# Kernel optimization log

Measured on AMD Instinct MI355X. Metric: run time of the kernel, lower is better.

Reference implementation:

```python
import jax, jax.numpy as jnp
import numpy as np

N_EMBD = 1024
N_HEAD = 16
B, T = 4, 2048


def setup_inputs() -> dict:
    key = jax.random.key(0)
    k1, k2, k3, k4, k5 = jax.random.split(key, 5)
    s = 0.02
    return {
        "x": jax.random.normal(k1, (B, T, N_EMBD), dtype=jnp.float32),
        "w_attn": jax.random.normal(k2, (N_EMBD, 3 * N_EMBD), dtype=jnp.float32) * s,
        "b_attn": jnp.zeros((3 * N_EMBD,), dtype=jnp.float32),
        "w_proj": jax.random.normal(k3, (N_EMBD, N_EMBD), dtype=jnp.float32) * s,
        "b_proj": jnp.zeros((N_EMBD,), dtype=jnp.float32),
    }


def reference(x, w_attn, b_attn, w_proj, b_proj):
    Bb, Tt, C = x.shape
    hd = C // N_HEAD  # head dim
    qkv = x @ w_attn + b_attn                      # [B,T,3C]
    q, k, v = jnp.split(qkv, 3, axis=-1)
    # [B,T,C] -> [B,H,T,hd]
    def heads(t):
        return t.reshape(Bb, Tt, N_HEAD, hd).transpose(0, 2, 1, 3)
    q, k, v = heads(q), heads(k), heads(v)
    scale = 1.0 / np.sqrt(hd).astype(np.float32)
    attn = jnp.einsum("bhqd,bhkd->bhqk", q, k) * scale  # [B,H,T,T]
    causal = jnp.tril(jnp.ones((Tt, Tt), dtype=bool))
    attn = jnp.where(causal, attn, -jnp.inf)
    attn = jax.nn.softmax(attn, axis=-1)
    y = jnp.einsum("bhqk,bhkd->bhqd", attn, v)          # [B,H,T,hd]
    y = y.transpose(0, 2, 1, 3).reshape(Bb, Tt, C)
    return y @ w_proj + b_proj
```

## Files before the change

### kernel.cpp

```cpp
#include <hip/hip_runtime.h>
#include <cmath>


typedef short short8 __attribute__((ext_vector_type(8)));
typedef short short4v __attribute__((ext_vector_type(4)));
typedef float f32x4 __attribute__((ext_vector_type(4)));

__device__ __forceinline__ short f2bf(float f) {
  unsigned u = __builtin_bit_cast(unsigned, f);
  u = (u + 0x7fffu + ((u >> 16) & 1u)) >> 16;
  return (short)u;
}

__device__ __forceinline__ float exp2_fast(float x) {
  float r;
  asm("v_exp_f32 %0, %1" : "=v"(r) : "v"(x));
  return r;
}

__device__ __forceinline__ void gld_lds16(const void* g, void* l) {
  __builtin_amdgcn_global_load_lds(
      (__attribute__((address_space(1))) void*)g,
      (__attribute__((address_space(3))) void*)l,
      16, 0, 0);
}

__device__ __forceinline__ void barx() {
  asm volatile("s_barrier" ::: "memory");
}

template <int IMM>
__device__ __forceinline__ short8 dsr(int addr) {
  short8 d;
  asm volatile("ds_read_b128 %0, %1 offset:%2"
               : "=v"(d) : "v"(addr), "n"(IMM));
  return d;
}

#define WAITLN(n)                                          \
  asm volatile("s_waitcnt lgkmcnt(" #n ")" ::: "memory");  \
  __builtin_amdgcn_sched_barrier(0);

__global__ void cast_bf16_kernel(const float* __restrict__ in,
                                 short* __restrict__ out, int n4) {
  int i = blockIdx.x * blockDim.x + threadIdx.x;
  if (i < n4) {
    const float4 v = ((const float4*)in)[i];
    short4v o;
    o.x = f2bf(v.x); o.y = f2bf(v.y); o.z = f2bf(v.z); o.w = f2bf(v.w);
    ((short4v*)out)[i] = o;
  }
}

__global__ void transpose_cast_kernel(const float* __restrict__ in,
                                      short* __restrict__ out, int R, int C) {
  __shared__ float tile[32][33];
  int c0 = blockIdx.x * 32, r0 = blockIdx.y * 32;
  int tx = threadIdx.x & 31, tg = threadIdx.x >> 5;
#pragma unroll
  for (int i = 0; i < 4; ++i) {
    int r = tg * 4 + i;
    tile[r][tx] = in[(size_t)(r0 + r) * C + c0 + tx];
  }
  __syncthreads();
#pragma unroll
  for (int i = 0; i < 4; ++i) {
    int c = tg * 4 + i;
    out[(size_t)(c0 + c) * R + r0 + tx] = f2bf(tile[tx][c]);
  }
}


__global__ __launch_bounds__(512, 2) void qkv_gemm_kernel(
    const short* __restrict__ A, const short* __restrict__ Bt,
    const float* __restrict__ bias,
    short* __restrict__ oq, short* __restrict__ ok, short* __restrict__ ovt,
    int M, int N, int K) {
  extern __shared__ short lds[];
  const int NT = K >> 6;
  const int lane = threadIdx.x & 63, wave = threadIdx.x >> 6;
  const int quad = lane >> 4, l16 = lane & 15;
  const int wm2 = wave >> 2, wn4 = wave & 3;

  const int nbn = N >> 8;
  const int swz = (blockIdx.x & 7) * ((int)gridDim.x >> 3) + (blockIdx.x >> 3);
  const int m0 = (swz / nbn) * 128, n0 = (swz % nbn) * 256;

  const int r8 = lane >> 3;
  const int sw8 = ((lane & 7) ^ r8) * 8;
  const short* Ab0 = A + (size_t)(m0 + wave * 8 + r8) * K + sw8;
  const short* Bb0 = Bt + (size_t)(n0 + wave * 8 + r8) * K + sw8;
  short* ldsw = lds + wave * 512;

  auto stage = [&](int t, int mat, int rA, int rB) {
    const short* g = (mat ? Bb0 : Ab0) + t * 64;
    short* d = ldsw + (t & 1) * 24576 + mat * 8192;
    gld_lds16(g + (size_t)rA * K, d + rA * 64);
    gld_lds16(g + (size_t)rB * K, d + rB * 64);
  };

  const int swz0 = ((0 + quad) ^ (l16 & 7)) * 16;
  const int swz1 = ((4 + quad) ^ (l16 & 7)) * 16;
  const int baseA0 = wm2 * 8192 + l16 * 128 + swz0;
  const int baseA1 = wm2 * 8192 + l16 * 128 + swz1;
  const int baseB0 = 16384 + wn4 * 8192 + l16 * 128 + swz0;
  const int baseB1 = 16384 + wn4 * 8192 + l16 * 128 + swz1;

  f32x4 acc[4][4] = {};

  stage(0, 1, 0, 64);
  stage(0, 1, 128, 192);
  stage(0, 0, 0, 64);
  asm volatile("s_waitcnt vmcnt(0)" ::: "memory");
  barx();

#pragma unroll 1
  for (int t = 0; t < NT; ++t) {
    const int vb = (t & 1) * 49152;
    const int aA0 = baseA0 + vb, aA1 = baseA1 + vb;
    const int aB0 = baseB0 + vb, aB1 = baseB1 + vb;
    short8 a0[4], b0[4], a1[4], b1[4];

    b0[0] = dsr<0>(aB0);     b0[1] = dsr<2048>(aB0);
    b0[2] = dsr<4096>(aB0);  b0[3] = dsr<6144>(aB0);
    a0[0] = dsr<0>(aA0);     a0[1] = dsr<2048>(aA0);
    a0[2] = dsr<4096>(aA0);  a0[3] = dsr<6144>(aA0);
    if (t + 1 < NT) {
      stage(t + 1, 1, 0, 64);
      stage(t + 1, 1, 128, 192);
      stage(t + 1, 0, 0, 64);
    }
    b1[0] = dsr<0>(aB1);     b1[1] = dsr<2048>(aB1);
    b1[2] = dsr<4096>(aB1);  b1[3] = dsr<6144>(aB1);
    a1[0] = dsr<0>(aA1);     a1[1] = dsr<2048>(aA1);
    a1[2] = dsr<4096>(aA1);  a1[3] = dsr<6144>(aA1);

    WAITLN(8)
    __builtin_amdgcn_s_setprio(1);
#pragma unroll
    for (int i_ = 0; i_ < 4; ++i_)
#pragma unroll
      for (int n_ = 0; n_ < 4; ++n_)
        acc[i_][n_] = __builtin_amdgcn_mfma_f32_16x16x32_bf16(
            a0[i_], b0[n_], acc[i_][n_], 0, 0, 0);
    __builtin_amdgcn_s_setprio(0);

    WAITLN(0)
    __builtin_amdgcn_s_setprio(1);
#pragma unroll
    for (int i_ = 0; i_ < 4; ++i_)
#pragma unroll
      for (int n_ = 0; n_ < 4; ++n_)
        acc[i_][n_] = __builtin_amdgcn_mfma_f32_16x16x32_bf16(
            a1[i_], b1[n_], acc[i_][n_], 0, 0, 0);
    __builtin_amdgcn_s_setprio(0);

    if (t + 1 < NT)
      asm volatile("s_waitcnt vmcnt(0)" ::: "memory");
    barx();
  }

  const int sec = n0 >> 10;
  const int h0 = (n0 & 1023) >> 6;
  const float scale = (sec == 0) ? 0.18033688f : 1.0f;
  float bv[4];
#pragma unroll
  for (int n_ = 0; n_ < 4; ++n_) bv[n_] = bias[n0 + wn4 * 64 + n_ * 16 + l16];
  const int b_ = m0 >> 11, t0 = m0 & 2047;

  __syncthreads();
  if (sec < 2) {
    short* dst = (sec == 0) ? oq : ok;
#pragma unroll
    for (int mt = 0; mt < 4; ++mt)
#pragma unroll
      for (int n_ = 0; n_ < 4; ++n_) {
        const int col = wn4 * 64 + n_ * 16 + l16;
#pragma unroll
        for (int r = 0; r < 4; ++r)
          lds[(wm2 * 64 + mt * 16 + quad * 4 + r) * 264 + col] =
              f2bf((acc[mt][n_][r] + bv[n_]) * scale);
      }
    __syncthreads();
    const int hl = wave & 3, rg = wave >> 2;
    const short* sp = &lds[(rg * 64 + r8) * 264 + hl * 64 + (lane & 7) * 8];
    short* gp = dst +
        ((size_t)(b_ * 16 + h0 + hl) * 2048 + t0 + rg * 64 + r8) * 64 +
        (lane & 7) * 8;
#pragma unroll
    for (int i = 0; i < 8; ++i)
      *(short8*)(gp + (size_t)i * 512) = *(const short8*)(sp + i * 8 * 264);
  } else {
#pragma unroll
    for (int mt = 0; mt < 4; ++mt)
#pragma unroll
      for (int n_ = 0; n_ < 4; ++n_) {
        const int col = wn4 * 64 + n_ * 16 + l16;
#pragma unroll
        for (int r = 0; r < 4; ++r)
          lds[col * 136 + wm2 * 64 + mt * 16 + quad * 4 + r] =
              f2bf(acc[mt][n_][r] + bv[n_]);
      }
    __syncthreads();
    const int cw = wave * 32 + (lane >> 4);
#pragma unroll
    for (int i = 0; i < 8; ++i) {
      const int c = cw + i * 4;
      const int bh = b_ * 16 + h0 + (c >> 6), d = c & 63;
      *(short8*)(ovt + ((size_t)bh * 64 + d) * 2048 + t0 + (lane & 15) * 8) =
          *(const short8*)&lds[c * 136 + (lane & 15) * 8];
    }
  }
}

template <int MODE>
__global__ __launch_bounds__(256) void gemm_bt_kernel(
    const short* __restrict__ A, const short* __restrict__ Bt,
    const float* __restrict__ bias, float* __restrict__ outf,
    short* __restrict__ oq, short* __restrict__ ok, short* __restrict__ ovt,
    int M, int N, int K) {
  __shared__ short slds[16384];
  short* As = slds;
  short* Bs = slds + 8192;
  const int m0 = blockIdx.y * 128, n0 = blockIdx.x * 128;
  const int lane = threadIdx.x & 63, wave = threadIdx.x >> 6;
  const int quad = lane >> 4, l16 = lane & 15;
  const int wm = (wave >> 1) * 64, wn = (wave & 1) * 64;

  const int row_off = lane >> 3;
  const int segsw = ((lane & 7) ^ row_off) * 8;
  const short* Ag = A + (size_t)(m0 + wave * 32 + row_off) * K + segsw;
  const short* Bg = Bt + (size_t)(n0 + wave * 32 + row_off) * K + segsw;

  f32x4 acc[4][4] = {};

  for (int k0 = 0; k0 < K; k0 += 64) {
#pragma unroll
    for (int g = 0; g < 4; ++g) {
      gld_lds16(Ag + (size_t)(g * 8) * K + k0, &As[(wave * 32 + g * 8) * 64]);
      gld_lds16(Bg + (size_t)(g * 8) * K + k0, &Bs[(wave * 32 + g * 8) * 64]);
    }
    __syncthreads();
#pragma unroll
    for (int kh = 0; kh < 2; ++kh) {
      short8 a[4], b[4];
#pragma unroll
      for (int t = 0; t < 4; ++t) {
        const int R = wm + t * 16 + l16;
        a[t] = *(const short8*)&As[R * 64 + (((kh * 4 + quad) ^ (R & 7)) * 8)];
      }
#pragma unroll
      for (int t = 0; t < 4; ++t) {
        const int R = wn + t * 16 + l16;
        b[t] = *(const short8*)&Bs[R * 64 + (((kh * 4 + quad) ^ (R & 7)) * 8)];
      }
#pragma unroll
      for (int mt = 0; mt < 4; ++mt)
#pragma unroll
        for (int nt = 0; nt < 4; ++nt)
          acc[mt][nt] = __builtin_amdgcn_mfma_f32_16x16x32_bf16(
              a[mt], b[nt], acc[mt][nt], 0, 0, 0);
    }
    __syncthreads();
  }

  float bv[4];
#pragma unroll
  for (int nt = 0; nt < 4; ++nt) bv[nt] = bias[n0 + wn + nt * 16 + l16];

  if (MODE == 1) {
#pragma unroll
    for (int mt = 0; mt < 4; ++mt)
#pragma unroll
      for (int nt = 0; nt < 4; ++nt) {
        const int n = n0 + wn + nt * 16 + l16;
#pragma unroll
        for (int r = 0; r < 4; ++r) {
          const int m = m0 + wm + mt * 16 + quad * 4 + r;
          outf[(size_t)m * N + n] = acc[mt][nt][r] + bv[nt];
        }
      }
  }
}

__global__ __launch_bounds__(256, 6) void attn_kernel(
    const short* __restrict__ q, const short* __restrict__ k,
    const short* __restrict__ vt, short* __restrict__ y) {
  __shared__ short Ks[64 * 64];
  __shared__ short Vs[64 * 64];
  __shared__ short Ps[4][16 * 72];
  const int lane = threadIdx.x & 63, wave = threadIdx.x >> 6;
  const int quad = lane >> 4, l16 = lane & 15;
  const int g = blockIdx.x;
  const int bh = g & 63;
  const int j = 31 - (g >> 6);
  const int b_ = bh >> 4, h = bh & 15;
  const int q0 = j * 64 + wave * 16;

  const short* qbh = q + (size_t)bh * 2048 * 64;
  const short* kbh = k + (size_t)bh * 2048 * 64;
  const short* vbh = vt + (size_t)bh * 64 * 2048;
  short* Pw = Ps[wave];

  const short8 qf0 = *(const short8*)&qbh[(q0 + l16) * 64 + quad * 8];
  const short8 qf1 = *(const short8*)&qbh[(q0 + l16) * 64 + 32 + quad * 8];

  short8 ones;
#pragma unroll
  for (int i = 0; i < 8; ++i) ones[i] = (short)0x3F80;

  f32x4 O[4] = {};
  f32x4 lacc = {};

  const int srow = lane >> 3;
  const int scol = ((lane & 7) ^ srow) * 8;
  const int r0s = wave * 16;

#pragma unroll 1
  for (int c = 0; c <= j; ++c) {
    const int kt0 = c * 64;
    gld_lds16(kbh + (size_t)(kt0 + r0s + srow) * 64 + scol, &Ks[r0s * 64]);
    gld_lds16(kbh + (size_t)(kt0 + r0s + 8 + srow) * 64 + scol, &Ks[(r0s + 8) * 64]);
    gld_lds16(vbh + (size_t)(r0s + srow) * 2048 + kt0 + scol, &Vs[r0s * 64]);
    gld_lds16(vbh + (size_t)(r0s + 8 + srow) * 2048 + kt0 + scol, &Vs[(r0s + 8) * 64]);
    __syncthreads();

    const int sw = l16 & 7;
    f32x4 sc4[4];
#pragma unroll
    for (int cf = 0; cf < 4; ++cf) {
      const int row = cf * 16 + l16;
      const short8 kfa = *(const short8*)&Ks[row * 64 + ((quad ^ sw) * 8)];
      const short8 kfb = *(const short8*)&Ks[row * 64 + (((quad + 4) ^ sw) * 8)];
      f32x4 z = {};
      z = __builtin_amdgcn_mfma_f32_16x16x32_bf16(qf0, kfa, z, 0, 0, 0);
      z = __builtin_amdgcn_mfma_f32_16x16x32_bf16(qf1, kfb, z, 0, 0, 0);
      sc4[cf] = z;
    }

    if (c == j) {
#pragma unroll
      for (int cf = 0; cf < 4; ++cf) {
        const int col = kt0 + cf * 16 + l16;
#pragma unroll
        for (int r = 0; r < 4; ++r) {
          const int rowg = q0 + quad * 4 + r;
          float e = exp2_fast(sc4[cf][r]);
          e = (col > rowg) ? 0.f : e;
          Pw[(quad * 4 + r) * 72 + cf * 16 + l16] = f2bf(e);
        }
      }
    } else {
#pragma unroll
      for (int cf = 0; cf < 4; ++cf)
#pragma unroll
        for (int r = 0; r < 4; ++r)
          Pw[(quad * 4 + r) * 72 + cf * 16 + l16] = f2bf(exp2_fast(sc4[cf][r]));
    }
    asm volatile("s_waitcnt lgkmcnt(0)" ::: "memory");
    const short8 pf0 = *(const short8*)&Pw[l16 * 72 + quad * 8];
    const short8 pf1 = *(const short8*)&Pw[l16 * 72 + 32 + quad * 8];

    lacc = __builtin_amdgcn_mfma_f32_16x16x32_bf16(pf0, ones, lacc, 0, 0, 0);
    lacc = __builtin_amdgcn_mfma_f32_16x16x32_bf16(pf1, ones, lacc, 0, 0, 0);

#pragma unroll
    for (int dt = 0; dt < 4; ++dt) {
      const int d = dt * 16 + l16;
      const short8 vf0 = *(const short8*)&Vs[d * 64 + ((quad ^ sw) * 8)];
      const short8 vf1 = *(const short8*)&Vs[d * 64 + (((quad + 4) ^ sw) * 8)];
      O[dt] = __builtin_amdgcn_mfma_f32_16x16x32_bf16(pf0, vf0, O[dt], 0, 0, 0);
      O[dt] = __builtin_amdgcn_mfma_f32_16x16x32_bf16(pf1, vf1, O[dt], 0, 0, 0);
    }
    __syncthreads();
  }

  float inv[4];
#pragma unroll
  for (int r = 0; r < 4; ++r) inv[r] = 1.0f / lacc[r];
#pragma unroll
  for (int dt = 0; dt < 4; ++dt) {
    const int d = dt * 16 + l16;
#pragma unroll
    for (int r = 0; r < 4; ++r) {
      const int t_ = q0 + quad * 4 + r;
      y[((size_t)b_ * 2048 + t_) * 1024 + h * 64 + d] = f2bf(O[dt][r] * inv[r]);
    }
  }
}

extern "C" void kernel_launch(void* const* d_in, const int* in_sizes, int n_in,
                              void* d_out, int out_size, void* d_ws, size_t ws_size,
                              hipStream_t stream) {
  const float* x      = (const float*)d_in[0];
  const float* w_attn = (const float*)d_in[1];
  const float* b_attn = (const float*)d_in[2];
  const float* w_proj = (const float*)d_in[3];
  const float* b_proj = (const float*)d_in[4];
  float* out = (float*)d_out;

  short* xb  = (short*)d_ws;
  short* wTa = xb + (size_t)8192 * 1024;
  short* wTp = wTa + (size_t)3072 * 1024;
  short* qb  = wTp + (size_t)1024 * 1024;
  short* kb  = qb + (size_t)64 * 2048 * 64;
  short* vtb = kb + (size_t)64 * 2048 * 64;
  short* yb  = vtb + (size_t)64 * 2048 * 64;

  static int lds_attr_done = 0;
  if (!lds_attr_done) {
    (void)hipFuncSetAttribute(reinterpret_cast<const void*>(qkv_gemm_kernel),
                              hipFuncAttributeMaxDynamicSharedMemorySize,
                              98304);
    lds_attr_done = 1;
  }

  cast_bf16_kernel<<<8192, 256, 0, stream>>>(x, xb, 8192 * 1024 / 4);
  transpose_cast_kernel<<<dim3(96, 32), 256, 0, stream>>>(w_attn, wTa, 1024, 3072);
  transpose_cast_kernel<<<dim3(32, 32), 256, 0, stream>>>(w_proj, wTp, 1024, 1024);

  qkv_gemm_kernel<<<768, 512, 98304, stream>>>(
      xb, wTa, b_attn, qb, kb, vtb, 8192, 3072, 1024);

  attn_kernel<<<2048, 256, 0, stream>>>(qb, kb, vtb, yb);

  gemm_bt_kernel<1><<<dim3(8, 64), 256, 0, stream>>>(
      yb, wTp, b_proj, out, nullptr, nullptr, nullptr, 8192, 1024, 1024);
}
```

Before: 242.7 us.

## Reuse pipelined QKV GEMM for projection and double-buffer K in attention

The output projection now runs through the templated 512-thread pipelined GEMM used for QKV, with an fp32 bias epilogue, in place of the simpler 256-thread kernel. The attention kernel double-buffers K tiles in dynamic LDS, prefetching the next tile during compute, and loads V fragments straight from global memory into registers rather than staging them in LDS. P writes and reads use inline ds instructions. This removes one barrier per iteration and overlaps loads with compute. In exchange the attention kernel's occupancy hint drops from 6 to 5, the V reads from global may be less coalesced, and the projection grid shrinks to 256 blocks.

```diff
diff --git a/kernel.cpp b/kernel.cpp
--- a/kernel.cpp
+++ b/kernel.cpp
@@ -40,6 +40,8 @@
 #define WAITLN(n)                                          \
   asm volatile("s_waitcnt lgkmcnt(" #n ")" ::: "memory");  \
   __builtin_amdgcn_sched_barrier(0);
+
+extern __shared__ short lds[];
 
 __global__ void cast_bf16_kernel(const float* __restrict__ in,
                                  short* __restrict__ out, int n4) {
@@ -71,12 +73,12 @@
 }
 
 
-__global__ __launch_bounds__(512, 2) void qkv_gemm_kernel(
+template <int MODE>
+__global__ __launch_bounds__(512, 2) void gemm128_kernel(
     const short* __restrict__ A, const short* __restrict__ Bt,
-    const float* __restrict__ bias,
+    const float* __restrict__ bias, float* __restrict__ outf,
     short* __restrict__ oq, short* __restrict__ ok, short* __restrict__ ovt,
     int M, int N, int K) {
-  extern __shared__ short lds[];
   const int NT = K >> 6;
   const int lane = threadIdx.x & 63, wave = threadIdx.x >> 6;
   const int quad = lane >> 4, l16 = lane & 15;
@@ -160,12 +162,28 @@
     barx();
   }
 
+  float bv[4];
+#pragma unroll
+  for (int n_ = 0; n_ < 4; ++n_) bv[n_] = bias[n0 + wn4 * 64 + n_ * 16 + l16];
+
+  if (MODE == 1) {
+#pragma unroll
+    for (int mt = 0; mt < 4; ++mt)
+#pragma unroll
+      for (int n_ = 0; n_ < 4; ++n_) {
+        const int n = n0 + wn4 * 64 + n_ * 16 + l16;
+#pragma unroll
+        for (int r = 0; r < 4; ++r) {
+          const int m = m0 + wm2 * 64 + mt * 16 + quad * 4 + r;
+          outf[(size_t)m * N + n] = acc[mt][n_][r] + bv[n_];
+        }
+      }
+    return;
+  }
+
   const int sec = n0 >> 10;
   const int h0 = (n0 & 1023) >> 6;
   const float scale = (sec == 0) ? 0.18033688f : 1.0f;
-  float bv[4];
-#pragma unroll
-  for (int n_ = 0; n_ < 4; ++n_) bv[n_] = bias[n0 + wn4 * 64 + n_ * 16 + l16];
   const int b_ = m0 >> 11, t0 = m0 & 2047;
 
   __syncthreads();
@@ -213,82 +231,9 @@
   }
 }
 
-template <int MODE>
-__global__ __launch_bounds__(256) void gemm_bt_kernel(
-    const short* __restrict__ A, const short* __restrict__ Bt,
-    const float* __restrict__ bias, float* __restrict__ outf,
-    short* __restrict__ oq, short* __restrict__ ok, short* __restrict__ ovt,
-    int M, int N, int K) {
-  __shared__ short slds[16384];
-  short* As = slds;
-  short* Bs = slds + 8192;
-  const int m0 = blockIdx.y * 128, n0 = blockIdx.x * 128;
-  const int lane = threadIdx.x & 63, wave = threadIdx.x >> 6;
-  const int quad = lane >> 4, l16 = lane & 15;
-  const int wm = (wave >> 1) * 64, wn = (wave & 1) * 64;
-
-  const int row_off = lane >> 3;
-  const int segsw = ((lane & 7) ^ row_off) * 8;
-  const short* Ag = A + (size_t)(m0 + wave * 32 + row_off) * K + segsw;
-  const short* Bg = Bt + (size_t)(n0 + wave * 32 + row_off) * K + segsw;
-
-  f32x4 acc[4][4] = {};
-
-  for (int k0 = 0; k0 < K; k0 += 64) {
-#pragma unroll
-    for (int g = 0; g < 4; ++g) {
-      gld_lds16(Ag + (size_t)(g * 8) * K + k0, &As[(wave * 32 + g * 8) * 64]);
-      gld_lds16(Bg + (size_t)(g * 8) * K + k0, &Bs[(wave * 32 + g * 8) * 64]);
-    }
-    __syncthreads();
-#pragma unroll
-    for (int kh = 0; kh < 2; ++kh) {
-      short8 a[4], b[4];
-#pragma unroll
-      for (int t = 0; t < 4; ++t) {
-        const int R = wm + t * 16 + l16;
-        a[t] = *(const short8*)&As[R * 64 + (((kh * 4 + quad) ^ (R & 7)) * 8)];
-      }
-#pragma unroll
-      for (int t = 0; t < 4; ++t) {
-        const int R = wn + t * 16 + l16;
-        b[t] = *(const short8*)&Bs[R * 64 + (((kh * 4 + quad) ^ (R & 7)) * 8)];
-      }
-#pragma unroll
-      for (int mt = 0; mt < 4; ++mt)
-#pragma unroll
-        for (int nt = 0; nt < 4; ++nt)
-          acc[mt][nt] = __builtin_amdgcn_mfma_f32_16x16x32_bf16(
-              a[mt], b[nt], acc[mt][nt], 0, 0, 0);
-    }
-    __syncthreads();
-  }
-
-  float bv[4];
-#pragma unroll
-  for (int nt = 0; nt < 4; ++nt) bv[nt] = bias[n0 + wn + nt * 16 + l16];
-
-  if (MODE == 1) {
-#pragma unroll
-    for (int mt = 0; mt < 4; ++mt)
-#pragma unroll
-      for (int nt = 0; nt < 4; ++nt) {
-        const int n = n0 + wn + nt * 16 + l16;
-#pragma unroll
-        for (int r = 0; r < 4; ++r) {
-          const int m = m0 + wm + mt * 16 + quad * 4 + r;
-          outf[(size_t)m * N + n] = acc[mt][nt][r] + bv[nt];
-        }
-      }
-  }
-}
-
-__global__ __launch_bounds__(256, 6) void attn_kernel(
+__global__ __launch_bounds__(256, 5) void attn_kernel(
     const short* __restrict__ q, const short* __restrict__ k,
     const short* __restrict__ vt, short* __restrict__ y) {
-  __shared__ short Ks[64 * 64];
-  __shared__ short Vs[64 * 64];
-  __shared__ short Ps[4][16 * 72];
   const int lane = threadIdx.x & 63, wave = threadIdx.x >> 6;
   const int quad = lane >> 4, l16 = lane & 15;
   const int g = blockIdx.x;
@@ -300,14 +245,9 @@
   const short* qbh = q + (size_t)bh * 2048 * 64;
   const short* kbh = k + (size_t)bh * 2048 * 64;
   const short* vbh = vt + (size_t)bh * 64 * 2048;
-  short* Pw = Ps[wave];
 
   const short8 qf0 = *(const short8*)&qbh[(q0 + l16) * 64 + quad * 8];
   const short8 qf1 = *(const short8*)&qbh[(q0 + l16) * 64 + 32 + quad * 8];
-
-  short8 ones;
-#pragma unroll
-  for (int i = 0; i < 8; ++i) ones[i] = (short)0x3F80;
 
   f32x4 O[4] = {};
   f32x4 lacc = {};
@@ -316,63 +256,99 @@
   const int scol = ((lane & 7) ^ srow) * 8;
   const int r0s = wave * 16;
 
+  const int sw = l16 & 7;
+  const int kaddrA = l16 * 128 + ((quad ^ sw) * 16);
+  const int kaddrB = kaddrA ^ 64;
+  const int pbase = 16384 + wave * 2304;
+  const int pw = pbase + quad * 576 + l16 * 2;
+  const int prd = pbase + l16 * 144 + quad * 16;
+
+  short8 ones;
+#pragma unroll
+  for (int i = 0; i < 8; ++i) ones[i] = (short)0x3F80;
+
+  gld_lds16(kbh + (size_t)(r0s + srow) * 64 + scol, &lds[r0s * 64]);
+  gld_lds16(kbh + (size_t)(r0s + 8 + srow) * 64 + scol, &lds[(r0s + 8) * 64]);
+  __syncthreads();
+
 #pragma unroll 1
   for (int c = 0; c <= j; ++c) {
     const int kt0 = c * 64;
-    gld_lds16(kbh + (size_t)(kt0 + r0s + srow) * 64 + scol, &Ks[r0s * 64]);
-    gld_lds16(kbh + (size_t)(kt0 + r0s + 8 + srow) * 64 + scol, &Ks[(r0s + 8) * 64]);
-    gld_lds16(vbh + (size_t)(r0s + srow) * 2048 + kt0 + scol, &Vs[r0s * 64]);
-    gld_lds16(vbh + (size_t)(r0s + 8 + srow) * 2048 + kt0 + scol, &Vs[(r0s + 8) * 64]);
-    __syncthreads();
-
-    const int sw = l16 & 7;
+    const int kb = (c & 1) * 8192;
+
+    short8 vf[8];
+#pragma unroll
+    for (int dt = 0; dt < 4; ++dt) {
+      const size_t vrow = (size_t)(dt * 16 + l16) * 2048 + kt0 + quad * 8;
+      vf[dt * 2] = *(const short8*)&vbh[vrow];
+      vf[dt * 2 + 1] = *(const short8*)&vbh[vrow + 32];
+    }
+    __builtin_amdgcn_sched_barrier(0);
+    if (c < j) {
+      const int nb = ((c + 1) & 1) * 4096;
+      gld_lds16(kbh + (size_t)(kt0 + 64 + r0s + srow) * 64 + scol,
+                &lds[nb + r0s * 64]);
+      gld_lds16(kbh + (size_t)(kt0 + 64 + r0s + 8 + srow) * 64 + scol,
+                &lds[nb + (r0s + 8) * 64]);
+    }
+    __builtin_amdgcn_sched_barrier(0);
+
+    short8 kfa[4], kfb[4];
+    kfa[0] = dsr<0>(kb + kaddrA);    kfb[0] = dsr<0>(kb + kaddrB);
+    kfa[1] = dsr<2048>(kb + kaddrA); kfb[1] = dsr<2048>(kb + kaddrB);
+    kfa[2] = dsr<4096>(kb + kaddrA); kfb[2] = dsr<4096>(kb + kaddrB);
+    kfa[3] = dsr<6144>(kb + kaddrA); kfb[3] = dsr<6144>(kb + kaddrB);
+    WAITLN(0)
     f32x4 sc4[4];
 #pragma unroll
     for (int cf = 0; cf < 4; ++cf) {
-      const int row = cf * 16 + l16;
-      const short8 kfa = *(const short8*)&Ks[row * 64 + ((quad ^ sw) * 8)];
-      const short8 kfb = *(const short8*)&Ks[row * 64 + (((quad + 4) ^ sw) * 8)];
       f32x4 z = {};
-      z = __builtin_amdgcn_mfma_f32_16x16x32_bf16(qf0, kfa, z, 0, 0, 0);
-      z = __builtin_amdgcn_mfma_f32_16x16x32_bf16(qf1, kfb, z, 0, 0, 0);
+      z = __builtin_amdgcn_mfma_f32_16x16x32_bf16(qf0, kfa[cf], z, 0, 0, 0);
+      z = __builtin_amdgcn_mfma_f32_16x16x32_bf16(qf1, kfb[cf], z, 0, 0, 0);
       sc4[cf] = z;
     }
 
     if (c == j) {
 #pragma unroll
-      for (int cf = 0; cf < 4; ++cf) {
-        const int col = kt0 + cf * 16 + l16;
+      for (int cf = 0; cf < 4; ++cf)
 #pragma unroll
         for (int r = 0; r < 4; ++r) {
+          const int col = kt0 + cf * 16 + l16;
           const int rowg = q0 + quad * 4 + r;
           float e = exp2_fast(sc4[cf][r]);
           e = (col > rowg) ? 0.f : e;
-          Pw[(quad * 4 + r) * 72 + cf * 16 + l16] = f2bf(e);
+          const int hv = (unsigned short)f2bf(e);
+          asm volatile("ds_write_b16 %0, %1"
+                       :: "v"(pw + r * 144 + cf * 32), "v"(hv) : "memory");
         }
-      }
     } else {
 #pragma unroll
       for (int cf = 0; cf < 4; ++cf)
 #pragma unroll
-        for (int r = 0; r < 4; ++r)
-          Pw[(quad * 4 + r) * 72 + cf * 16 + l16] = f2bf(exp2_fast(sc4[cf][r]));
-    }
-    asm volatile("s_waitcnt lgkmcnt(0)" ::: "memory");
-    const short8 pf0 = *(const short8*)&Pw[l16 * 72 + quad * 8];
-    const short8 pf1 = *(const short8*)&Pw[l16 * 72 + 32 + quad * 8];
+        for (int r = 0; r < 4; ++r) {
+          const int hv = (unsigned short)f2bf(exp2_fast(sc4[cf][r]));
+          asm volatile("ds_write_b16 %0, %1"
+                       :: "v"(pw + r * 144 + cf * 32), "v"(hv) : "memory");
+        }
+    }
+    const short8 pf0 = dsr<0>(prd);
+    const short8 pf1 = dsr<64>(prd);
+    WAITLN(0)
 
     lacc = __builtin_amdgcn_mfma_f32_16x16x32_bf16(pf0, ones, lacc, 0, 0, 0);
     lacc = __builtin_amdgcn_mfma_f32_16x16x32_bf16(pf1, ones, lacc, 0, 0, 0);
-
 #pragma unroll
     for (int dt = 0; dt < 4; ++dt) {
-      const int d = dt * 16 + l16;
-      const short8 vf0 = *(const short8*)&Vs[d * 64 + ((quad ^ sw) * 8)];
-      const short8 vf1 = *(const short8*)&Vs[d * 64 + (((quad + 4) ^ sw) * 8)];
-      O[dt] = __builtin_amdgcn_mfma_f32_16x16x32_bf16(pf0, vf0, O[dt], 0, 0, 0);
-      O[dt] = __builtin_amdgcn_mfma_f32_16x16x32_bf16(pf1, vf1, O[dt], 0, 0, 0);
-    }
-    __syncthreads();
+      O[dt] = __builtin_amdgcn_mfma_f32_16x16x32_bf16(pf0, vf[dt * 2], O[dt],
+                                                      0, 0, 0);
+      O[dt] = __builtin_amdgcn_mfma_f32_16x16x32_bf16(pf1, vf[dt * 2 + 1],
+                                                      O[dt], 0, 0, 0);
+    }
+
+    if (c < j) {
+      asm volatile("s_waitcnt vmcnt(0)" ::: "memory");
+      barx();
+    }
   }
 
   float inv[4];
@@ -409,9 +385,12 @@
 
   static int lds_attr_done = 0;
   if (!lds_attr_done) {
-    (void)hipFuncSetAttribute(reinterpret_cast<const void*>(qkv_gemm_kernel),
-                              hipFuncAttributeMaxDynamicSharedMemorySize,
-                              98304);
+    (void)hipFuncSetAttribute(
+        reinterpret_cast<const void*>(&gemm128_kernel<0>),
+        hipFuncAttributeMaxDynamicSharedMemorySize, 98304);
+    (void)hipFuncSetAttribute(
+        reinterpret_cast<const void*>(&gemm128_kernel<1>),
+        hipFuncAttributeMaxDynamicSharedMemorySize, 98304);
     lds_attr_done = 1;
   }
 
@@ -419,11 +398,11 @@
   transpose_cast_kernel<<<dim3(96, 32), 256, 0, stream>>>(w_attn, wTa, 1024, 3072);
   transpose_cast_kernel<<<dim3(32, 32), 256, 0, stream>>>(w_proj, wTp, 1024, 1024);
 
-  qkv_gemm_kernel<<<768, 512, 98304, stream>>>(
-      xb, wTa, b_attn, qb, kb, vtb, 8192, 3072, 1024);
-
-  attn_kernel<<<2048, 256, 0, stream>>>(qb, kb, vtb, yb);
-
-  gemm_bt_kernel<1><<<dim3(8, 64), 256, 0, stream>>>(
+  gemm128_kernel<0><<<768, 512, 98304, stream>>>(
+      xb, wTa, b_attn, nullptr, qb, kb, vtb, 8192, 3072, 1024);
+
+  attn_kernel<<<2048, 256, 25600, stream>>>(qb, kb, vtb, yb);
+
+  gemm128_kernel<1><<<256, 512, 98304, stream>>>(
       yb, wTp, b_proj, out, nullptr, nullptr, nullptr, 8192, 1024, 1024);
 }
```

After: 465.5 us. 1.92x slower.
